# Kernel optimization log

Measured on AMD Instinct MI355X. Metric: run time of the kernel, lower is better.

Reference implementation:

```python
import jax, jax.numpy as jnp
import numpy as np
from jax import lax

VOCAB, EMB, H, L, B = 32000, 512, 512, 256, 64


def _flip_bwd(t):
    # t: (L, B, 2, ...); reverse time for the backward direction (dir index 1)
    return jnp.stack([t[:, :, 0], t[::-1, :, 1]], axis=2)


def sru_layer(x, W, bias, k, n_out):
    """Bidirectional SRU layer.
    x: (L, B, n_in); W: (n_in, 2*n_out*k); bias: (2, 2, n_out) = (gate{f,r}, dir, n_out).
    k=4: 4th projection is the highway input; k=3: highway uses x itself (n_in == 2*n_out).
    """
    Lx, Bx, _ = x.shape
    u = (x @ W).reshape(Lx, Bx, 2, n_out, k)
    u = _flip_bwd(u)  # both directions now scan forward in time
    f = jax.nn.sigmoid(u[..., 1] + bias[0][None, None])  # (L,B,2,n_out)
    r = jax.nn.sigmoid(u[..., 2] + bias[1][None, None])
    x_tilde = u[..., 0]

    def step(c, inp):
        f_t, xt = inp
        c = f_t * c + (1.0 - f_t) * xt
        return c, c

    c0 = jnp.zeros((Bx, 2, n_out), x.dtype)
    c_last, cs = lax.scan(step, c0, (f, x_tilde))

    if k == 4:
        x_res = u[..., 3]
    else:
        x_res = _flip_bwd(x.reshape(Lx, Bx, 2, n_out))
    h = r * jnp.tanh(cs) + (1.0 - r) * x_res
    h = _flip_bwd(h)  # restore true time order for backward dir
    return h.reshape(Lx, Bx, 2 * n_out), c_last.reshape(Bx, 2 * n_out)


def setup_inputs() -> dict:
    key = jax.random.key(0)
    ks = jax.random.split(key, 8)
    inp = {
        'padded_encoder_inputs': jax.random.randint(ks[0], (L, B), 0, VOCAB),
        'emb': jax.random.normal(ks[1], (VOCAB, EMB), jnp.float32) * 0.1,
        'W0': jax.random.normal(ks[2], (EMB, 2 * H * 4), jnp.float32) * 0.05,
        'b0': jax.random.normal(ks[3], (2, 2, H), jnp.float32) * 0.05,
        'W1': jax.random.normal(ks[4], (2 * H, 2 * H * 3), jnp.float32) * 0.05,
        'b1': jax.random.normal(ks[5], (2, 2, H), jnp.float32) * 0.05,
        'Wd': jax.random.normal(ks[6], (H, 2 * H), jnp.float32) * 0.05,
        'bd': jax.random.normal(ks[7], (H,), jnp.float32) * 0.05,
    }
    return inp


def reference(padded_encoder_inputs, emb, W0, b0, W1, b1, Wd, bd):
    # embedding lookup (dropout layers are identity in eval mode)
    x = emb[padded_encoder_inputs]            # (L, B, EMB)
    h1, c1 = sru_layer(x, W0, b0, 4, H)       # (L,B,2H), (B,2H)
    h2, c2 = sru_layer(h1, W1, b1, 3, H)
    hidden = jnp.stack([c1, c2], axis=0)      # (layers, B, 2H)
    hidden = hidden @ Wd.T + bd               # dense_hidden: (layers, B, H)
    return h2, hidden
```

## Files before the change

kernel.cpp:

```cpp
#include <hip/hip_runtime.h>

typedef __attribute__((ext_vector_type(8))) short bf16x8;
typedef __attribute__((ext_vector_type(4))) float f32x4;

__device__ __forceinline__ float b2f(ushort s) { return __uint_as_float(((uint)s) << 16); }
__device__ __forceinline__ ushort f2b(float f) {
  uint u = __float_as_uint(f);
  u += 0x7fff + ((u >> 16) & 1);
  return (ushort)(u >> 16);
}

__device__ __forceinline__ void store_h(float* p, float v) { *p = v; }
__device__ __forceinline__ void store_h(ushort* p, float v) { *p = f2b(v); }

__device__ __forceinline__ float sigm_fast(float x) { return 1.f / (1.f + __expf(-x)); }
__device__ __forceinline__ float tanh_fast(float c) {
  float e = __expf(-2.f * fabsf(c));
  float t = (1.f - e) / (1.f + e);
  return copysignf(t, c);
}

__global__ void transpose_kernel(const float* __restrict__ in, ushort* __restrict__ out,
                                 int R, int C) {
  __shared__ ushort tile[32][33];
  int bc = blockIdx.x << 5;
  int br = blockIdx.y << 5;
  int tx = threadIdx.x & 31;
  int ty = threadIdx.x >> 5;
#pragma unroll
  for (int i = 0; i < 32; i += 8)
    tile[ty + i][tx] = f2b(in[(size_t)(br + ty + i) * C + bc + tx]);
  __syncthreads();
#pragma unroll
  for (int i = 0; i < 32; i += 8)
    out[(size_t)(bc + ty + i) * R + br + tx] = tile[tx][ty + i];
}

__global__ void embed_kernel(const int* __restrict__ tok, const float* __restrict__ emb,
                             ushort* __restrict__ x) {
  int tid = threadIdx.x;
  int r = (blockIdx.x << 2) + (tid >> 6);
  int c = (tid & 63) << 3;
  int t = tok[r];
  const float* src = emb + ((size_t)t << 9) + c;
  float4 a = *(const float4*)src;
  float4 b = *(const float4*)(src + 4);
  uint4 o;
  o.x = (uint)f2b(a.x) | ((uint)f2b(a.y) << 16);
  o.y = (uint)f2b(a.z) | ((uint)f2b(a.w) << 16);
  o.z = (uint)f2b(b.x) | ((uint)f2b(b.y) << 16);
  o.w = (uint)f2b(b.z) | ((uint)f2b(b.w) << 16);
  *(uint4*)(x + ((size_t)r << 9) + c) = o;
}

__global__ __launch_bounds__(512) void gemm_bt3_kernel(
    const ushort* __restrict__ A, const ushort* __restrict__ BT,
    ushort* __restrict__ C, int M, int N, int K) {
  __shared__ char lds[2][65536];
  const int tid = threadIdx.x;
  const int lane = tid & 63;
  const int wave = tid >> 6;
  const int wr = wave >> 2;
  const int wc = wave & 3;

  const int xcd = blockIdx.x & 7;
  const int l = blockIdx.x >> 3;
  const int s = xcd * (gridDim.x >> 8) + (l >> 5);
  const int uu = l & 31;
  const int mt = ((s & 7) << 3) + (uu & 7);
  const int nt = ((s >> 3) << 2) + (uu >> 3);
  const int m0 = mt << 8;
  const int n0 = nt << 8;
  const int NT = K >> 6;

  auto stage = [&](int t, int p) {
    const ushort* Asrc = A + (size_t)m0 * K + (t << 6);
    const ushort* Bsrc = BT + (size_t)n0 * K + (t << 6);
#pragma unroll
    for (int i = 0; i < 8; ++i) {
      int sub = i & 3;
      int off = (sub << 13) + (tid << 4);
      int row = off >> 7;
      int col = ((off & 127) ^ ((row & 7) << 4)) >> 1;
      const ushort* src = ((i < 4) ? Asrc : Bsrc) + (size_t)row * K + col;
      char* dst = lds[p] + ((i < 4) ? 0 : 32768) + (sub << 13) + (wave << 10);
      __builtin_amdgcn_global_load_lds(
          (const __attribute__((address_space(1))) void*)src,
          (__attribute__((address_space(3))) void*)dst, 16, 0, 0);
    }
  };

  f32x4 acc[8][4];
#pragma unroll
  for (int i = 0; i < 8; ++i)
#pragma unroll
    for (int j = 0; j < 4; ++j) acc[i][j] = (f32x4){0.f, 0.f, 0.f, 0.f};

  stage(0, 0);
  for (int t = 0; t < NT; ++t) {
    int p = t & 1;
    if (t + 1 < NT) {
      stage(t + 1, p ^ 1);
      asm volatile("s_waitcnt vmcnt(8)" ::: "memory");
    } else {
      asm volatile("s_waitcnt vmcnt(0)" ::: "memory");
    }
    __builtin_amdgcn_s_barrier();
    const char* base = (const char*)lds[p];
#pragma unroll
    for (int kk = 0; kk < 2; ++kk) {
      const int kof2 = ((kk << 5) + ((lane >> 4) << 3)) << 1;
      bf16x8 af[8], bg[4];
#pragma unroll
      for (int mi = 0; mi < 8; ++mi) {
        int row = (wr << 7) + (mi << 4) + (lane & 15);
        int byte = (row << 7) + kof2;
        byte ^= (row & 7) << 4;
        af[mi] = *(const bf16x8*)(base + byte);
      }
#pragma unroll
      for (int ni = 0; ni < 4; ++ni) {
        int row = (wc << 6) + (ni << 4) + (lane & 15);
        int byte = (row << 7) + kof2;
        byte ^= (row & 7) << 4;
        bg[ni] = *(const bf16x8*)(base + 32768 + byte);
      }
      __builtin_amdgcn_s_setprio(1);
#pragma unroll
      for (int mi = 0; mi < 8; ++mi)
#pragma unroll
        for (int ni = 0; ni < 4; ++ni)
          acc[mi][ni] =
              __builtin_amdgcn_mfma_f32_16x16x32_bf16(af[mi], bg[ni], acc[mi][ni], 0, 0, 0);
      __builtin_amdgcn_s_setprio(0);
    }
    __builtin_amdgcn_s_barrier();
  }
#pragma unroll
  for (int mi = 0; mi < 8; ++mi) {
#pragma unroll
    for (int j = 0; j < 4; ++j) {
      int row = m0 + (wr << 7) + (mi << 4) + ((lane >> 4) << 2) + j;
      size_t bofs = (size_t)row * N + n0 + (wc << 6);
#pragma unroll
      for (int ni = 0; ni < 4; ++ni)
        C[bofs + (ni << 4) + (lane & 15)] = f2b(acc[mi][ni][j]);
    }
  }
}

template <int KC, typename OT>
__global__ void sru_scan_kernel(const ushort* __restrict__ u, const float* __restrict__ bias,
                                const ushort* __restrict__ xres, OT* __restrict__ hout,
                                float* __restrict__ cout) {
  const int L = 256, B = 64, H = 512;
  int idx = blockIdx.x * 256 + threadIdx.x;
  int h = idx & (H - 1);
  int dir = (idx >> 9) & 1;
  int b = idx >> 10;
  float bfg = bias[dir * H + h];
  float brg = bias[2 * H + dir * H + h];
  const size_t ustep = (size_t)B * 2 * H * KC;
  const ushort* ubase = u + ((size_t)b * 2 + dir) * H * KC + (size_t)h * KC;
  const size_t hstep = (size_t)B * 2 * H;
  const size_t hoff = (size_t)b * 2 * H + (size_t)dir * H + h;
  float c = 0.f;
#pragma unroll 16
  for (int s = 0; s < L; ++s) {
    int t = dir ? (L - 1 - s) : s;
    const ushort* up = ubase + (size_t)t * ustep;
    float xt, fg, rg, xr;
    if (KC == 4) {
      uint2 v = *(const uint2*)up;
      xt = b2f((ushort)(v.x & 0xffff));
      fg = b2f((ushort)(v.x >> 16));
      rg = b2f((ushort)(v.y & 0xffff));
      xr = b2f((ushort)(v.y >> 16));
    } else {
      xt = b2f(up[0]);
      fg = b2f(up[1]);
      rg = b2f(up[2]);
      xr = b2f(xres[hoff + (size_t)t * hstep]);
    }
    float f = sigm_fast(fg + bfg);
    float r = sigm_fast(rg + brg);
    c = f * c + (1.f - f) * xt;
    float hv = r * tanh_fast(c) + (1.f - r) * xr;
    store_h(hout + hoff + (size_t)t * hstep, hv);
  }
  cout[(size_t)b * 2 * H + (size_t)dir * H + h] = c;
}

__global__ __launch_bounds__(512) void dense_kernel(
    const float* __restrict__ c12, const ushort* __restrict__ WdT,
    const float* __restrict__ bd, float* __restrict__ out) {
  int row = blockIdx.x;
  int j = threadIdx.x;
  const float* c = c12 + (size_t)row * 1024;
  float acc = bd[j];
#pragma unroll 8
  for (int k = 0; k < 1024; ++k) acc += c[k] * b2f(WdT[(size_t)k * 512 + j]);
  out[(size_t)row * 512 + j] = acc;
}

extern "C" void kernel_launch(void* const* d_in, const int* in_sizes, int n_in,
                              void* d_out, int out_size, void* d_ws, size_t ws_size,
                              hipStream_t stream) {
  const int* tok = (const int*)d_in[0];
  const float* emb = (const float*)d_in[1];
  const float* W0 = (const float*)d_in[2];
  const float* b0 = (const float*)d_in[3];
  const float* W1 = (const float*)d_in[4];
  const float* b1 = (const float*)d_in[5];
  const float* Wd = (const float*)d_in[6];
  const float* bd = (const float*)d_in[7];
  float* out = (float*)d_out;

  char* ws = (char*)d_ws;
  ushort* x = (ushort*)ws;
  ushort* W0T = (ushort*)(ws + 16777216);
  ushort* W1T = (ushort*)(ws + 20971520);
  ushort* u = (ushort*)(ws + 27262976);
  ushort* h1 = (ushort*)(ws + 161480704);
  float* c12 = (float*)(ws + 195035136);
  ushort* WdT = (ushort*)(ws + 27262976 + 100663296);

  transpose_kernel<<<dim3(128, 16), 256, 0, stream>>>(W0, W0T, 512, 4096);
  transpose_kernel<<<dim3(96, 32), 256, 0, stream>>>(W1, W1T, 1024, 3072);
  embed_kernel<<<4096, 256, 0, stream>>>(tok, emb, x);
  gemm_bt3_kernel<<<1024, 512, 0, stream>>>(x, W0T, u, 16384, 4096, 512);
  sru_scan_kernel<4, ushort><<<256, 256, 0, stream>>>(u, b0, (const ushort*)nullptr, h1, c12);
  gemm_bt3_kernel<<<768, 512, 0, stream>>>(h1, W1T, u, 16384, 3072, 1024);
  sru_scan_kernel<3, float><<<256, 256, 0, stream>>>(u, b1, h1, out, c12 + 65536);
  transpose_kernel<<<dim3(32, 16), 256, 0, stream>>>(Wd, WdT, 512, 1024);
  dense_kernel<<<128, 512, 0, stream>>>(c12, WdT, bd, out + 16777216);
}
```

Measured before the change: 371.8 us.

## Deepen GEMM pipeline to four LDS stages with 32-wide K tiles

```diff
diff --git a/kernel.cpp b/kernel.cpp
--- a/kernel.cpp
+++ b/kernel.cpp
@@ -53,10 +53,10 @@
   *(uint4*)(x + ((size_t)r << 9) + c) = o;
 }
 
-__global__ __launch_bounds__(512) void gemm_bt3_kernel(
+__global__ __launch_bounds__(512, 1) void gemm_bt7_kernel(
     const ushort* __restrict__ A, const ushort* __restrict__ BT,
     ushort* __restrict__ C, int M, int N, int K) {
-  __shared__ char lds[2][65536];
+  __shared__ char lds[4][32768];
   const int tid = threadIdx.x;
   const int lane = tid & 63;
   const int wave = tid >> 6;
@@ -71,19 +71,27 @@
   const int nt = ((s >> 3) << 2) + (uu >> 3);
   const int m0 = mt << 8;
   const int n0 = nt << 8;
-  const int NT = K >> 6;
+  const int NT = K >> 5;
+
+  const int aBase = (wr << 13) + ((lane & 15) << 6) + ((lane >> 4) << 4);
+  const int bBase = 16384 + (wc << 12) + ((lane & 15) << 6) + ((lane >> 4) << 4);
+
+  int srcoff[2];
+#pragma unroll
+  for (int sub = 0; sub < 2; ++sub) {
+    int row = (sub << 7) + (wave << 4) + (lane >> 2);
+    srcoff[sub] = row * K + ((lane & 3) << 3);
+  }
+  const ushort* Abase = A + (size_t)m0 * K;
+  const ushort* Bbase = BT + (size_t)n0 * K;
 
   auto stage = [&](int t, int p) {
-    const ushort* Asrc = A + (size_t)m0 * K + (t << 6);
-    const ushort* Bsrc = BT + (size_t)n0 * K + (t << 6);
-#pragma unroll
-    for (int i = 0; i < 8; ++i) {
-      int sub = i & 3;
-      int off = (sub << 13) + (tid << 4);
-      int row = off >> 7;
-      int col = ((off & 127) ^ ((row & 7) << 4)) >> 1;
-      const ushort* src = ((i < 4) ? Asrc : Bsrc) + (size_t)row * K + col;
-      char* dst = lds[p] + ((i < 4) ? 0 : 32768) + (sub << 13) + (wave << 10);
+    const int tk = t << 5;
+#pragma unroll
+    for (int i = 0; i < 4; ++i) {
+      int sub = i & 1;
+      const ushort* src = ((i < 2) ? Abase : Bbase) + srcoff[sub] + tk;
+      char* dst = lds[p] + ((i < 2) ? 0 : 16384) + (sub << 13) + (wave << 10);
       __builtin_amdgcn_global_load_lds(
           (const __attribute__((address_space(1))) void*)src,
           (__attribute__((address_space(3))) void*)dst, 16, 0, 0);
@@ -97,45 +105,37 @@
     for (int j = 0; j < 4; ++j) acc[i][j] = (f32x4){0.f, 0.f, 0.f, 0.f};
 
   stage(0, 0);
+  stage(1, 1);
+  stage(2, 2);
+
   for (int t = 0; t < NT; ++t) {
-    int p = t & 1;
-    if (t + 1 < NT) {
-      stage(t + 1, p ^ 1);
+    if (t < NT - 2) {
       asm volatile("s_waitcnt vmcnt(8)" ::: "memory");
+    } else if (t == NT - 2) {
+      asm volatile("s_waitcnt vmcnt(4)" ::: "memory");
     } else {
       asm volatile("s_waitcnt vmcnt(0)" ::: "memory");
     }
     __builtin_amdgcn_s_barrier();
-    const char* base = (const char*)lds[p];
-#pragma unroll
-    for (int kk = 0; kk < 2; ++kk) {
-      const int kof2 = ((kk << 5) + ((lane >> 4) << 3)) << 1;
-      bf16x8 af[8], bg[4];
-#pragma unroll
-      for (int mi = 0; mi < 8; ++mi) {
-        int row = (wr << 7) + (mi << 4) + (lane & 15);
-        int byte = (row << 7) + kof2;
-        byte ^= (row & 7) << 4;
-        af[mi] = *(const bf16x8*)(base + byte);
-      }
-#pragma unroll
-      for (int ni = 0; ni < 4; ++ni) {
-        int row = (wc << 6) + (ni << 4) + (lane & 15);
-        int byte = (row << 7) + kof2;
-        byte ^= (row & 7) << 4;
-        bg[ni] = *(const bf16x8*)(base + 32768 + byte);
-      }
-      __builtin_amdgcn_s_setprio(1);
-#pragma unroll
-      for (int mi = 0; mi < 8; ++mi)
-#pragma unroll
-        for (int ni = 0; ni < 4; ++ni)
-          acc[mi][ni] =
-              __builtin_amdgcn_mfma_f32_16x16x32_bf16(af[mi], bg[ni], acc[mi][ni], 0, 0, 0);
-      __builtin_amdgcn_s_setprio(0);
-    }
-    __builtin_amdgcn_s_barrier();
-  }
+    if (t + 3 < NT) stage(t + 3, (t + 3) & 3);
+
+    const char* base = (const char*)lds[0] + ((t & 3) << 15);
+    bf16x8 af[8], bg[4];
+    af[0] = *(const bf16x8*)(base + aBase);
+#pragma unroll
+    for (int ni = 0; ni < 4; ++ni) bg[ni] = *(const bf16x8*)(base + bBase + (ni << 10));
+#pragma unroll
+    for (int mi = 1; mi < 8; ++mi) af[mi] = *(const bf16x8*)(base + aBase + (mi << 10));
+    __builtin_amdgcn_s_setprio(1);
+#pragma unroll
+    for (int mi = 0; mi < 8; ++mi)
+#pragma unroll
+      for (int ni = 0; ni < 4; ++ni)
+        acc[mi][ni] =
+            __builtin_amdgcn_mfma_f32_16x16x32_bf16(af[mi], bg[ni], acc[mi][ni], 0, 0, 0);
+    __builtin_amdgcn_s_setprio(0);
+  }
+
 #pragma unroll
   for (int mi = 0; mi < 8; ++mi) {
 #pragma unroll
@@ -228,9 +228,9 @@
   transpose_kernel<<<dim3(128, 16), 256, 0, stream>>>(W0, W0T, 512, 4096);
   transpose_kernel<<<dim3(96, 32), 256, 0, stream>>>(W1, W1T, 1024, 3072);
   embed_kernel<<<4096, 256, 0, stream>>>(tok, emb, x);
-  gemm_bt3_kernel<<<1024, 512, 0, stream>>>(x, W0T, u, 16384, 4096, 512);
+  gemm_bt7_kernel<<<1024, 512, 0, stream>>>(x, W0T, u, 16384, 4096, 512);
   sru_scan_kernel<4, ushort><<<256, 256, 0, stream>>>(u, b0, (const ushort*)nullptr, h1, c12);
-  gemm_bt3_kernel<<<768, 512, 0, stream>>>(h1, W1T, u, 16384, 3072, 1024);
+  gemm_bt7_kernel<<<768, 512, 0, stream>>>(h1, W1T, u, 16384, 3072, 1024);
   sru_scan_kernel<3, float><<<256, 256, 0, stream>>>(u, b1, h1, out, c12 + 65536);
   transpose_kernel<<<dim3(32, 16), 256, 0, stream>>>(Wd, WdT, 512, 1024);
   dense_kernel<<<128, 512, 0, stream>>>(c12, WdT, bd, out + 16777216);
```

Result: no change. 374.6 us (+0.8%).
